# Performance work log

Hardware: AMD Instinct MI355X
Metric: run time of the kernel (lower is better)

The kernel has to match this reference:

```python
import jax, jax.numpy as jnp
import numpy as np

N, IN_F, OUT_F = 65536, 512, 512


def setup_inputs() -> dict:
    key = jax.random.key(0)
    k1, k2, k3 = jax.random.split(key, 3)
    # Activations arrive as dequant-pending uint8-valued floats in [0, 256).
    x = jax.random.randint(k1, (N, IN_F), 0, 256).astype(jnp.float32)
    weight = jax.random.randint(k2, (OUT_F, IN_F), 0, 256).astype(jnp.int32)
    bias = jax.random.randint(k3, (OUT_F,), -512, 512).astype(jnp.int32)
    return {
        "x": x,
        "weight": weight,
        "bias": bias,
        "M": jnp.asarray(0.0123, dtype=jnp.float32),
        "x_zero": jnp.asarray(128.0, dtype=jnp.float32),
        "w_zero": jnp.asarray(128.0, dtype=jnp.float32),
        "y_zero": jnp.asarray(128.0, dtype=jnp.float32),
    }


def reference(x, weight, bias, M, x_zero, w_zero, y_zero):
    # y = round(linear(x - x_zero, w - w_zero, b) * M + y_zero)
    xs = x - x_zero                                   # [N, IN_F]
    w = weight.astype(jnp.float32) - w_zero           # [OUT_F, IN_F]
    y = jnp.einsum("ni,oi->no", xs, w) + bias.astype(jnp.float32)
    return jnp.round(y * M + y_zero)
```

## Files before the change

### kernel.cpp

```cpp
#include <hip/hip_runtime.h>


#define K_DIM 512
#define OUTF  512
#define NT    8
#define LDAB  80
#define A_BYTES (128 * LDAB)
#define B_OFF   A_BYTES
#define BUF_B   (A_BYTES + 16 * 1024)

typedef __attribute__((ext_vector_type(4))) int   i32x4;
typedef __attribute__((ext_vector_type(4))) float f32x4;

__device__ __forceinline__ void gload16(const void* g, void* l) {
    __builtin_amdgcn_global_load_lds(
        (const __attribute__((address_space(1))) void*)g,
        (__attribute__((address_space(3))) void*)l, 16, 0, 0);
}

__global__ void wprep(const int* __restrict__ W, unsigned int* __restrict__ Wb,
                      const float* __restrict__ wzp) {
    const int wz = __float2int_rn(wzp[0]);
    int idx = (blockIdx.x * blockDim.x + threadIdx.x) * 4;
    i32x4 w = *reinterpret_cast<const i32x4*>(W + idx);
    unsigned int p = ((unsigned int)(w[0] - wz) & 0xffu)
                   | (((unsigned int)(w[1] - wz) & 0xffu) << 8)
                   | (((unsigned int)(w[2] - wz) & 0xffu) << 16)
                   | (((unsigned int)(w[3] - wz) & 0xffu) << 24);
    Wb[idx >> 2] = p;
}

__global__ __launch_bounds__(512, 4)
void qgemm(const float* __restrict__ X,
           const unsigned char* __restrict__ Wb,
           const int* __restrict__ bias,
           const float* __restrict__ Mp,
           const float* __restrict__ xzp,
           const float* __restrict__ yzp,
           float* __restrict__ Y) {
    __shared__ unsigned char lds[2][BUF_B];

    const int tid  = threadIdx.x;
    const int lane = tid & 63;
    const int wid  = tid >> 6;
    const int wr   = wid >> 2;
    const int wc   = wid & 3;
    const int fr   = lane & 15;
    const int fq   = lane >> 4;

    const int b = blockIdx.x;
    const int lid = (b & 7) * 128 + (b >> 3);
    const int row0 = (lid >> 1) * 128;
    const int n0   = (lid & 1) * 256;

    const float xzf = xzp[0];

    const int srow = tid >> 2;
    const float* xbase = X + (size_t)(row0 + srow) * K_DIM + (tid & 3) * 16;
    const int aoff = srow * LDAB + (tid & 3) * 16;

    const unsigned char* wbase = Wb + (size_t)(n0 + wid * 32 + fr) * K_DIM + fq * 16;
    const int ldsB = B_OFF + wid * 2048;

    f32x4 ra[2][4];

    auto stageA = [&](int t) {
        const int s = t & 1;
        const float* xp = xbase + t * 64;
        #pragma unroll
        for (int q = 0; q < 4; ++q)
            ra[s][q] = *reinterpret_cast<const f32x4*>(xp + q * 4);
    };
    auto gloadB = [&](int t, int buf) {
        const unsigned char* g = wbase + t * 64;
        gload16(g,               &lds[buf][ldsB]);
        gload16(g + 16 * K_DIM,  &lds[buf][ldsB + 1024]);
    };
    auto convwriteA = [&](int t) {
        const int s = t & 1;
        i32x4 pa;
        #pragma unroll
        for (int q = 0; q < 4; ++q) {
            unsigned int u0 = (unsigned int)((int)(ra[s][q][0] - xzf)) & 0xffu;
            unsigned int u1 = (unsigned int)((int)(ra[s][q][1] - xzf)) & 0xffu;
            unsigned int u2 = (unsigned int)((int)(ra[s][q][2] - xzf)) & 0xffu;
            unsigned int u3 = (unsigned int)((int)(ra[s][q][3] - xzf)) & 0xffu;
            pa[q] = (int)(u0 | (u1 << 8) | (u2 << 16) | (u3 << 24));
        }
        *reinterpret_cast<i32x4*>(&lds[s][aoff]) = pa;
    };

    const int c0 = n0 + wc * 64;
    i32x4 acc[4][4];
    #pragma unroll
    for (int n = 0; n < 4; ++n) {
        const int bv = bias[c0 + n * 16 + fr];
        #pragma unroll
        for (int m = 0; m < 4; ++m)
            acc[m][n] = i32x4{bv, bv, bv, bv};
    }

    const int aro = (wr * 64 + fr) * LDAB + fq * 16;

    auto compute = [&](int t) {
        const int s = t & 1;
        i32x4 bf[4];
        #pragma unroll
        for (int n = 0; n < 4; ++n)
            bf[n] = *reinterpret_cast<const i32x4*>(&lds[s][B_OFF + (wc * 4 + n) * 1024 + lane * 16]);
        #pragma unroll
        for (int m = 0; m < 4; ++m) {
            i32x4 af = *reinterpret_cast<const i32x4*>(&lds[s][aro + m * 16 * LDAB]);
            #pragma unroll
            for (int n = 0; n < 4; ++n)
                acc[m][n] = __builtin_amdgcn_mfma_i32_16x16x64_i8(
                    af, bf[n], acc[m][n], 0, 0, 0);
        }
    };

    stageA(0);
    stageA(1);
    gloadB(0, 0);
    convwriteA(0);
    __syncthreads();

    #pragma unroll
    for (int t = 0; t < NT; ++t) {
        if (t + 2 < NT) stageA(t + 2);
        if (t + 1 < NT) gloadB(t + 1, (t + 1) & 1);
        compute(t);
        if (t + 1 < NT) convwriteA(t + 1);
        __syncthreads();
    }

    const float Mv = Mp[0], yz = yzp[0];
    #pragma unroll
    for (int n = 0; n < 4; ++n) {
        const int col = c0 + n * 16 + fr;
        #pragma unroll
        for (int m = 0; m < 4; ++m) {
            const int row = row0 + wr * 64 + m * 16 + fq * 4;
            float* yp = Y + (size_t)row * OUTF + col;
            #pragma unroll
            for (int j = 0; j < 4; ++j)
                yp[(size_t)j * OUTF] = rintf((float)acc[m][n][j] * Mv + yz);
        }
    }
}

extern "C" void kernel_launch(void* const* d_in, const int* in_sizes, int n_in,
                              void* d_out, int out_size, void* d_ws, size_t ws_size,
                              hipStream_t stream) {
    const float* x    = (const float*)d_in[0];
    const int*   w    = (const int*)d_in[1];
    const int*   bias = (const int*)d_in[2];
    const float* M    = (const float*)d_in[3];
    const float* xz   = (const float*)d_in[4];
    const float* wz   = (const float*)d_in[5];
    const float* yz   = (const float*)d_in[6];
    float* y = (float*)d_out;

    unsigned int* Wb = (unsigned int*)d_ws;

    wprep<<<256, 256, 0, stream>>>(w, Wb, wz);
    qgemm<<<1024, 512, 0, stream>>>(x, (const unsigned char*)Wb, bias, M, xz, yz, y);
}
```

Measured before the change: 67.98 us.

## Retile int8 GEMM to 64-row blocks spanning all output columns

Each block now computes a 64×512 output tile instead of 128×256, so every fp32 activation row is read from global memory once rather than by two blocks. The A tile in LDS is stored directly in MFMA-fragment order, so each wave reads its fragments with plain lane-strided loads and the padded row layout is dropped. Each wave now computes a 2×8 grid of MFMA tiles. In exchange, each block loads all 512 weight rows per K step, which doubles per-block LDS use and weight traffic from L2 and may lower the number of resident blocks per CU.

```diff
diff --git a/kernel.cpp b/kernel.cpp
--- a/kernel.cpp
+++ b/kernel.cpp
@@ -4,13 +4,12 @@
 #define K_DIM 512
 #define OUTF  512
 #define NT    8
-#define LDAB  80
-#define A_BYTES (128 * LDAB)
-#define B_OFF   A_BYTES
-#define BUF_B   (A_BYTES + 16 * 1024)
+#define B_OFF 4096
+#define BUF_B (4096 + 32768)
 
 typedef __attribute__((ext_vector_type(4))) int   i32x4;
 typedef __attribute__((ext_vector_type(4))) float f32x4;
+typedef __attribute__((ext_vector_type(2))) unsigned int u32x2;
 
 __device__ __forceinline__ void gload16(const void* g, void* l) {
     __builtin_amdgcn_global_load_lds(
@@ -48,73 +47,68 @@
     const int fr   = lane & 15;
     const int fq   = lane >> 4;
 
-    const int b = blockIdx.x;
-    const int lid = (b & 7) * 128 + (b >> 3);
-    const int row0 = (lid >> 1) * 128;
-    const int n0   = (lid & 1) * 256;
+    const int row0 = blockIdx.x * 64;
 
     const float xzf = xzp[0];
 
-    const int srow = tid >> 2;
-    const float* xbase = X + (size_t)(row0 + srow) * K_DIM + (tid & 3) * 16;
-    const int aoff = srow * LDAB + (tid & 3) * 16;
+    const int arow  = tid >> 3;
+    const int kslot = tid & 7;
+    const float* xbase = X + (size_t)(row0 + arow) * K_DIM + kslot * 8;
+    const int dA = (arow >> 4) * 1024 + (((arow & 15) + ((kslot >> 1) << 4)) << 4)
+                 + ((kslot & 1) << 3);
 
-    const unsigned char* wbase = Wb + (size_t)(n0 + wid * 32 + fr) * K_DIM + fq * 16;
-    const int ldsB = B_OFF + wid * 2048;
+    const unsigned char* wbase = Wb + (size_t)(wid * 64 + fr) * K_DIM + fq * 16;
+    const int ldsB = B_OFF + wid * 4096;
 
-    f32x4 ra[2][4];
+    f32x4 ra[2][2];
 
     auto stageA = [&](int t) {
         const int s = t & 1;
-        const float* xp = xbase + t * 64;
-        #pragma unroll
-        for (int q = 0; q < 4; ++q)
-            ra[s][q] = *reinterpret_cast<const f32x4*>(xp + q * 4);
+        const float* p = xbase + t * 64;
+        ra[s][0] = *reinterpret_cast<const f32x4*>(p);
+        ra[s][1] = *reinterpret_cast<const f32x4*>(p + 4);
     };
     auto gloadB = [&](int t, int buf) {
         const unsigned char* g = wbase + t * 64;
-        gload16(g,               &lds[buf][ldsB]);
-        gload16(g + 16 * K_DIM,  &lds[buf][ldsB + 1024]);
+        #pragma unroll
+        for (int f = 0; f < 4; ++f)
+            gload16(g + (size_t)f * 16 * K_DIM, &lds[buf][ldsB + f * 1024]);
     };
     auto convwriteA = [&](int t) {
         const int s = t & 1;
-        i32x4 pa;
+        u32x2 v;
         #pragma unroll
-        for (int q = 0; q < 4; ++q) {
-            unsigned int u0 = (unsigned int)((int)(ra[s][q][0] - xzf)) & 0xffu;
-            unsigned int u1 = (unsigned int)((int)(ra[s][q][1] - xzf)) & 0xffu;
-            unsigned int u2 = (unsigned int)((int)(ra[s][q][2] - xzf)) & 0xffu;
-            unsigned int u3 = (unsigned int)((int)(ra[s][q][3] - xzf)) & 0xffu;
-            pa[q] = (int)(u0 | (u1 << 8) | (u2 << 16) | (u3 << 24));
+        for (int h = 0; h < 2; ++h) {
+            unsigned int u0 = (unsigned int)((int)(ra[s][h][0] - xzf)) & 0xffu;
+            unsigned int u1 = (unsigned int)((int)(ra[s][h][1] - xzf)) & 0xffu;
+            unsigned int u2 = (unsigned int)((int)(ra[s][h][2] - xzf)) & 0xffu;
+            unsigned int u3 = (unsigned int)((int)(ra[s][h][3] - xzf)) & 0xffu;
+            v[h] = u0 | (u1 << 8) | (u2 << 16) | (u3 << 24);
         }
-        *reinterpret_cast<i32x4*>(&lds[s][aoff]) = pa;
+        *reinterpret_cast<u32x2*>(&lds[s][dA]) = v;
     };
 
-    const int c0 = n0 + wc * 64;
-    i32x4 acc[4][4];
+    const int c0 = wc * 128;
+    i32x4 acc[2][8];
     #pragma unroll
-    for (int n = 0; n < 4; ++n) {
+    for (int n = 0; n < 8; ++n) {
         const int bv = bias[c0 + n * 16 + fr];
-        #pragma unroll
-        for (int m = 0; m < 4; ++m)
-            acc[m][n] = i32x4{bv, bv, bv, bv};
+        acc[0][n] = i32x4{bv, bv, bv, bv};
+        acc[1][n] = i32x4{bv, bv, bv, bv};
     }
 
-    const int aro = (wr * 64 + fr) * LDAB + fq * 16;
+    const int aBase = (wr * 2) * 1024 + lane * 16;
+    const int bBase = B_OFF + (wc * 8) * 1024 + lane * 16;
 
     auto compute = [&](int t) {
         const int s = t & 1;
-        i32x4 bf[4];
+        i32x4 af0 = *reinterpret_cast<const i32x4*>(&lds[s][aBase]);
+        i32x4 af1 = *reinterpret_cast<const i32x4*>(&lds[s][aBase + 1024]);
         #pragma unroll
-        for (int n = 0; n < 4; ++n)
-            bf[n] = *reinterpret_cast<const i32x4*>(&lds[s][B_OFF + (wc * 4 + n) * 1024 + lane * 16]);
-        #pragma unroll
-        for (int m = 0; m < 4; ++m) {
-            i32x4 af = *reinterpret_cast<const i32x4*>(&lds[s][aro + m * 16 * LDAB]);
-            #pragma unroll
-            for (int n = 0; n < 4; ++n)
-                acc[m][n] = __builtin_amdgcn_mfma_i32_16x16x64_i8(
-                    af, bf[n], acc[m][n], 0, 0, 0);
+        for (int n = 0; n < 8; ++n) {
+            i32x4 bf = *reinterpret_cast<const i32x4*>(&lds[s][bBase + n * 1024]);
+            acc[0][n] = __builtin_amdgcn_mfma_i32_16x16x64_i8(af0, bf, acc[0][n], 0, 0, 0);
+            acc[1][n] = __builtin_amdgcn_mfma_i32_16x16x64_i8(af1, bf, acc[1][n], 0, 0, 0);
         }
     };
 
@@ -135,12 +129,11 @@
 
     const float Mv = Mp[0], yz = yzp[0];
     #pragma unroll
-    for (int n = 0; n < 4; ++n) {
-        const int col = c0 + n * 16 + fr;
+    for (int m = 0; m < 2; ++m) {
+        const int row = row0 + wr * 32 + m * 16 + fq * 4;
         #pragma unroll
-        for (int m = 0; m < 4; ++m) {
-            const int row = row0 + wr * 64 + m * 16 + fq * 4;
-            float* yp = Y + (size_t)row * OUTF + col;
+        for (int n = 0; n < 8; ++n) {
+            float* yp = Y + (size_t)row * OUTF + c0 + n * 16 + fr;
             #pragma unroll
             for (int j = 0; j < 4; ++j)
                 yp[(size_t)j * OUTF] = rintf((float)acc[m][n][j] * Mv + yz);
```

New measurement: 74.67 us. 9.8% more time.

## Keep full weight slice resident in LDS and stream 16-row activation chunks

Applied to the files above, without the earlier changes.

The GEMM is restructured so each block loads its entire 256x512 int8 weight slice into LDS once (128KB). It then streams the activation tile in 16-row chunks across the full K, with each wave computing a 16x32 output per chunk and writing results immediately. This removes the per-K-step weight reloads and keeps fewer accumulators. The cost is much larger LDS use, which limits occupancy to one block per CU, and less MFMA work per LDS read since the A fragment is shared over only two B tiles.

```diff
diff --git a/kernel.cpp b/kernel.cpp
--- a/kernel.cpp
+++ b/kernel.cpp
@@ -3,11 +3,8 @@
 
 #define K_DIM 512
 #define OUTF  512
-#define NT    8
-#define LDAB  80
-#define A_BYTES (128 * LDAB)
-#define B_OFF   A_BYTES
-#define BUF_B   (A_BYTES + 16 * 1024)
+#define W_LDS  131072
+#define A_OFF  W_LDS
 
 typedef __attribute__((ext_vector_type(4))) int   i32x4;
 typedef __attribute__((ext_vector_type(4))) float f32x4;
@@ -30,7 +27,7 @@
     Wb[idx >> 2] = p;
 }
 
-__global__ __launch_bounds__(512, 4)
+__global__ __launch_bounds__(512, 1)
 void qgemm(const float* __restrict__ X,
            const unsigned char* __restrict__ Wb,
            const int* __restrict__ bias,
@@ -38,46 +35,47 @@
            const float* __restrict__ xzp,
            const float* __restrict__ yzp,
            float* __restrict__ Y) {
-    __shared__ unsigned char lds[2][BUF_B];
+    __shared__ unsigned char lds[W_LDS + 2 * 8192];
 
     const int tid  = threadIdx.x;
     const int lane = tid & 63;
     const int wid  = tid >> 6;
-    const int wr   = wid >> 2;
-    const int wc   = wid & 3;
     const int fr   = lane & 15;
     const int fq   = lane >> 4;
 
-    const int b = blockIdx.x;
+    const int b   = blockIdx.x;
     const int lid = (b & 7) * 128 + (b >> 3);
+    const int n0  = (lid & 1) * 256;
     const int row0 = (lid >> 1) * 128;
-    const int n0   = (lid & 1) * 256;
 
     const float xzf = xzp[0];
 
-    const int srow = tid >> 2;
-    const float* xbase = X + (size_t)(row0 + srow) * K_DIM + (tid & 3) * 16;
-    const int aoff = srow * LDAB + (tid & 3) * 16;
+    {
+        const unsigned char* wg = Wb + (size_t)(n0 + wid * 32 + fr) * K_DIM + fq * 16;
+        #pragma unroll
+        for (int nn = 0; nn < 2; ++nn)
+            #pragma unroll
+            for (int t = 0; t < 8; ++t)
+                gload16(wg + (size_t)nn * 16 * K_DIM + t * 64,
+                        &lds[(((2 * wid + nn) * 8 + t) << 10)]);
+    }
 
-    const unsigned char* wbase = Wb + (size_t)(n0 + wid * 32 + fr) * K_DIM + fq * 16;
-    const int ldsB = B_OFF + wid * 2048;
+    const int arow = tid & 15;
+    const int ak   = ((tid >> 6) << 6) + (((tid >> 4) & 3) << 4);
+    const float* xbase = X + (size_t)(row0 + arow) * K_DIM + ak;
+    const int dA = tid * 16;
 
     f32x4 ra[2][4];
 
-    auto stageA = [&](int t) {
-        const int s = t & 1;
-        const float* xp = xbase + t * 64;
+    auto stageA = [&](int c) {
+        const int s = c & 1;
+        const float* p = xbase + (size_t)c * 16 * K_DIM;
         #pragma unroll
         for (int q = 0; q < 4; ++q)
-            ra[s][q] = *reinterpret_cast<const f32x4*>(xp + q * 4);
+            ra[s][q] = *reinterpret_cast<const f32x4*>(p + q * 4);
     };
-    auto gloadB = [&](int t, int buf) {
-        const unsigned char* g = wbase + t * 64;
-        gload16(g,               &lds[buf][ldsB]);
-        gload16(g + 16 * K_DIM,  &lds[buf][ldsB + 1024]);
-    };
-    auto convwriteA = [&](int t) {
-        const int s = t & 1;
+    auto convwriteA = [&](int c) {
+        const int s = c & 1;
         i32x4 pa;
         #pragma unroll
         for (int q = 0; q < 4; ++q) {
@@ -87,64 +85,48 @@
             unsigned int u3 = (unsigned int)((int)(ra[s][q][3] - xzf)) & 0xffu;
             pa[q] = (int)(u0 | (u1 << 8) | (u2 << 16) | (u3 << 24));
         }
-        *reinterpret_cast<i32x4*>(&lds[s][aoff]) = pa;
+        *reinterpret_cast<i32x4*>(&lds[A_OFF + s * 8192 + dA]) = pa;
     };
 
-    const int c0 = n0 + wc * 64;
-    i32x4 acc[4][4];
-    #pragma unroll
-    for (int n = 0; n < 4; ++n) {
-        const int bv = bias[c0 + n * 16 + fr];
-        #pragma unroll
-        for (int m = 0; m < 4; ++m)
-            acc[m][n] = i32x4{bv, bv, bv, bv};
-    }
+    const int col0 = n0 + wid * 32 + fr;
+    const int bv0 = bias[col0];
+    const int bv1 = bias[col0 + 16];
 
-    const int aro = (wr * 64 + fr) * LDAB + fq * 16;
+    const float Mv = Mp[0], yz = yzp[0];
 
-    auto compute = [&](int t) {
-        const int s = t & 1;
-        i32x4 bf[4];
-        #pragma unroll
-        for (int n = 0; n < 4; ++n)
-            bf[n] = *reinterpret_cast<const i32x4*>(&lds[s][B_OFF + (wc * 4 + n) * 1024 + lane * 16]);
-        #pragma unroll
-        for (int m = 0; m < 4; ++m) {
-            i32x4 af = *reinterpret_cast<const i32x4*>(&lds[s][aro + m * 16 * LDAB]);
-            #pragma unroll
-            for (int n = 0; n < 4; ++n)
-                acc[m][n] = __builtin_amdgcn_mfma_i32_16x16x64_i8(
-                    af, bf[n], acc[m][n], 0, 0, 0);
-        }
-    };
+    const int bOff0 = ((2 * wid)     * 8) << 10;
+    const int bOff1 = ((2 * wid + 1) * 8) << 10;
 
     stageA(0);
-    stageA(1);
-    gloadB(0, 0);
     convwriteA(0);
     __syncthreads();
 
     #pragma unroll
-    for (int t = 0; t < NT; ++t) {
-        if (t + 2 < NT) stageA(t + 2);
-        if (t + 1 < NT) gloadB(t + 1, (t + 1) & 1);
-        compute(t);
-        if (t + 1 < NT) convwriteA(t + 1);
+    for (int c = 0; c < 8; ++c) {
+        if (c + 1 < 8) stageA(c + 1);
+
+        const int ab = A_OFF + (c & 1) * 8192;
+        i32x4 acc0 = {bv0, bv0, bv0, bv0};
+        i32x4 acc1 = {bv1, bv1, bv1, bv1};
+        #pragma unroll
+        for (int t = 0; t < 8; ++t) {
+            i32x4 af = *reinterpret_cast<const i32x4*>(&lds[ab + (t << 10) + lane * 16]);
+            i32x4 bf0 = *reinterpret_cast<const i32x4*>(&lds[bOff0 + (t << 10) + lane * 16]);
+            i32x4 bf1 = *reinterpret_cast<const i32x4*>(&lds[bOff1 + (t << 10) + lane * 16]);
+            acc0 = __builtin_amdgcn_mfma_i32_16x16x64_i8(af, bf0, acc0, 0, 0, 0);
+            acc1 = __builtin_amdgcn_mfma_i32_16x16x64_i8(af, bf1, acc1, 0, 0, 0);
+        }
+
+        const int row = row0 + c * 16 + fq * 4;
+        float* yp = Y + (size_t)row * OUTF + col0;
+        #pragma unroll
+        for (int j = 0; j < 4; ++j) {
+            yp[(size_t)j * OUTF]      = rintf((float)acc0[j] * Mv + yz);
+            yp[(size_t)j * OUTF + 16] = rintf((float)acc1[j] * Mv + yz);
+        }
+
+        if (c + 1 < 8) convwriteA(c + 1);
         __syncthreads();
-    }
-
-    const float Mv = Mp[0], yz = yzp[0];
-    #pragma unroll
-    for (int n = 0; n < 4; ++n) {
-        const int col = c0 + n * 16 + fr;
-        #pragma unroll
-        for (int m = 0; m < 4; ++m) {
-            const int row = row0 + wr * 64 + m * 16 + fq * 4;
-            float* yp = Y + (size_t)row * OUTF + col;
-            #pragma unroll
-            for (int j = 0; j < 4; ++j)
-                yp[(size_t)j * OUTF] = rintf((float)acc[m][n][j] * Mv + yz);
-        }
     }
 }
 
```

After: 87.51 us. 28.7% more time.
